# Kernel tuning notes

Hardware: AMD Instinct MI355X
Metric: run time of the kernel (lower is better)

The kernel has to match this reference:

```python
import jax, jax.numpy as jnp
import numpy as np

EPS = 1e-8


def setup_inputs() -> dict:
    key = jax.random.key(0)
    student_output = jax.random.normal(key, (8192, 768), dtype=jnp.float32)
    return {"student_output": student_output}


def reference(student_output) -> jnp.ndarray:
    # F.normalize(x, p=2, dim=-1, eps): x / max(||x||, eps)
    norm = jnp.linalg.norm(student_output, axis=-1, keepdims=True)
    x = student_output / jnp.maximum(norm, EPS)  # [B, D]

    # Brute-force 1-NN via max inner product (vectors are L2-normalized)
    dots = x @ x.T  # [B, B]
    n = x.shape[0]
    dots = dots.at[jnp.arange(n), jnp.arange(n)].set(-1.0)  # mask self
    indices = jnp.argmax(dots, axis=1)  # [B]

    # torch.nn.PairwiseDistance(2, eps): ||x1 - x2 + eps||_2
    diff = x - x[indices] + EPS  # [B, D]
    distances = jnp.sqrt(jnp.sum(diff * diff, axis=-1))  # [B]

    loss = -jnp.mean(jnp.log(distances + EPS))
    return loss
```

## Files before the change

### kernel.cpp

```cpp
#include <hip/hip_runtime.h>
#include <math.h>

#define NB 8192
#define D 768
#define EPSV 1e-8f
#define BT 256
#define BK 64
#define NT (NB / BT)
#define NBLK (NT * (NT + 1) / 2)

typedef float f32x4 __attribute__((ext_vector_type(4)));
typedef short s16x8 __attribute__((ext_vector_type(8)));

#define BARM() asm volatile("s_barrier" ::: "memory")
#define LGKM0() asm volatile("s_waitcnt lgkmcnt(0)" ::: "memory")
#define VMC(n) asm volatile("s_waitcnt vmcnt(" #n ")" ::: "memory")

__device__ __forceinline__ unsigned short f2bf(float f) {
  unsigned u = __float_as_uint(f);
  u += 0x7fffu + ((u >> 16) & 1u);
  return (unsigned short)(u >> 16);
}
__device__ __forceinline__ unsigned encf(float f) {
  unsigned u = __float_as_uint(f);
  return (u & 0x80000000u) ? ~u : (u | 0x80000000u);
}
__device__ __forceinline__ float decf(unsigned u) {
  return (u & 0x80000000u) ? __uint_as_float(u & 0x7fffffffu)
                           : __uint_as_float(~u);
}
__device__ __forceinline__ void mfma_bf16(f32x4& c, s16x8 a, s16x8 b) {
  c = __builtin_amdgcn_mfma_f32_16x16x32_bf16(a, b, c, 0, 0, 0);
}

__device__ __forceinline__ int swz(int p) { return p ^ (((p >> 7) & 7) << 4); }

__device__ __forceinline__ void stage_half(const unsigned short* __restrict__ xb,
                                           unsigned short* lds, int rbase,
                                           int row0, int k0, int w, int l) {
#pragma unroll
  for (int i = 0; i < 2; ++i) {
    const int pu = i * 8192 + w * 1024;
    const int p = pu + l * 16;
    const int sp = swz(p);
    const unsigned short* src =
        xb + (size_t)(row0 + (sp >> 7)) * D + k0 + ((sp & 127) >> 1);
    __builtin_amdgcn_global_load_lds(
        (const __attribute__((address_space(1))) void*)src,
        (__attribute__((address_space(3))) void*)(lds + rbase + (pu >> 1)), 16,
        0, 0);
  }
}

__device__ __forceinline__ s16x8 ldfrag(const unsigned short* lds, int rbase,
                                        int r, int c) {
  const int b = swz((r << 7) | (c << 1));
  return *(const s16x8*)(lds + rbase + (b >> 1));
}

__global__ __launch_bounds__(256) void normalize_kernel(
    const float* __restrict__ in, unsigned short* __restrict__ xb) {
  const int row = blockIdx.x;
  const int t = threadIdx.x;
  float4 v = make_float4(0.f, 0.f, 0.f, 0.f);
  const float4* rp = (const float4*)(in + (size_t)row * D);
  if (t < D / 4) v = rp[t];
  float ss = v.x * v.x + v.y * v.y + v.z * v.z + v.w * v.w;
#pragma unroll
  for (int m = 1; m < 64; m <<= 1) ss += __shfl_xor(ss, m, 64);
  __shared__ float wss[4];
  if ((t & 63) == 0) wss[t >> 6] = ss;
  __syncthreads();
  float tot = wss[0] + wss[1] + wss[2] + wss[3];
  float inv = 1.0f / fmaxf(sqrtf(tot), EPSV);
  if (t < D / 4) {
    ushort4 o;
    o.x = f2bf(v.x * inv);
    o.y = f2bf(v.y * inv);
    o.z = f2bf(v.z * inv);
    o.w = f2bf(v.w * inv);
    *(ushort4*)(xb + (size_t)row * D + t * 4) = o;
  }
}

__global__ __launch_bounds__(512) void gemm_max_kernel(
    const unsigned short* __restrict__ xb, unsigned* __restrict__ gmax) {
  __shared__ unsigned short lds[65536];
  const int t = threadIdx.x;
  const int w = t >> 6, l = t & 63;
  const int wm = w >> 2, wn = w & 3;

  const int bid = blockIdx.x;
  const int widx = (bid & 7) * (NBLK / 8) + (bid >> 3);
  int brow = (int)((sqrtf(8.0f * (float)widx + 1.0f) - 1.0f) * 0.5f);
  while ((brow + 1) * (brow + 2) / 2 <= widx) ++brow;
  while (brow * (brow + 1) / 2 > widx) --brow;
  const int bcol = widx - brow * (brow + 1) / 2;
  const bool diag = (brow == bcol);
  const int arow = brow * BT, acol = bcol * BT;

  f32x4 acc[8][4] = {};

  const int AB = wm * 8192;
  const int BB = 16384 + (wn >> 1) * 8192;

#define RD_B(buf)                                                             \
  {                                                                           \
    _Pragma("unroll") for (int n = 0; n < 4; ++n) _Pragma("unroll") for (     \
        int kk = 0; kk < 2;                                                   \
        ++kk) bfr[n * 2 + kk] = ldfrag(lds, (buf) + BB,                       \
                                       (wn & 1) * 64 + n * 16 + (l & 15),     \
                                       kk * 32 + (l >> 4) * 8);               \
  }
#define RD_A(buf, dst, m0)                                                    \
  {                                                                           \
    _Pragma("unroll") for (int mm = 0; mm < 2; ++mm) _Pragma("unroll") for (  \
        int kk = 0; kk < 2;                                                   \
        ++kk) dst[mm * 2 + kk] = ldfrag(lds, (buf) + AB,                      \
                                        ((m0) + mm) * 16 + (l & 15),          \
                                        kk * 32 + (l >> 4) * 8);              \
  }
#define MFMA_Q(q, a)                                                          \
  {                                                                           \
    __builtin_amdgcn_s_setprio(1);                                            \
    _Pragma("unroll") for (int mm = 0; mm < 2; ++mm)                          \
        _Pragma("unroll") for (int n = 0; n < 4; ++n)                         \
            _Pragma("unroll") for (int kk = 0; kk < 2; ++kk)                  \
                mfma_bf16(acc[2 * (q) + mm][n], a[mm * 2 + kk],               \
                          bfr[n * 2 + kk]);                                   \
    __builtin_amdgcn_s_setprio(0);                                            \
  }

  stage_half(xb, lds, 0, arow, 0, w, l);
  stage_half(xb, lds, 8192, arow + 128, 0, w, l);
  stage_half(xb, lds, 16384, acol, 0, w, l);
  stage_half(xb, lds, 24576, acol + 128, 0, w, l);
  VMC(4);
  stage_half(xb, lds, 32768 + 16384, acol, 64, w, l);
  stage_half(xb, lds, 32768 + 24576, acol + 128, 64, w, l);
  stage_half(xb, lds, 32768, arow, 64, w, l);
  VMC(6);
  BARM();

#pragma unroll 1
  for (int itn = 0; itn < 6; ++itn) {
    const int kC1 = 2 * itn + 1;
    const int kS0 = (2 * itn + 2 < 12) ? 2 * itn + 2 : 11;
    const int kS1 = (2 * itn + 3 < 12) ? 2 * itn + 3 : 11;
    s16x8 bfr[8], aA[4], aB[4], aC[4], aD[4];

    RD_B(0);
    RD_A(0, aA, 0);
    stage_half(xb, lds, 32768 + 8192, arow + 128, kC1 * 64, w, l);
    BARM();
    LGKM0();
    MFMA_Q(0, aA);
    BARM();

    RD_A(0, aB, 2);
    RD_A(0, aC, 4);
    stage_half(xb, lds, 16384, acol, kS0 * 64, w, l);
    BARM();
    LGKM0();
    MFMA_Q(1, aB);
    BARM();

    RD_A(0, aD, 6);
    stage_half(xb, lds, 24576, acol + 128, kS0 * 64, w, l);
    BARM();
    LGKM0();
    MFMA_Q(2, aC);
    BARM();

    stage_half(xb, lds, 0, arow, kS0 * 64, w, l);
    BARM();
    LGKM0();
    MFMA_Q(3, aD);
    VMC(6);
    BARM();

    RD_B(32768);
    RD_A(32768, aA, 0);
    stage_half(xb, lds, 8192, arow + 128, kS0 * 64, w, l);
    BARM();
    LGKM0();
    MFMA_Q(0, aA);
    BARM();

    RD_A(32768, aB, 2);
    RD_A(32768, aC, 4);
    stage_half(xb, lds, 32768 + 16384, acol, kS1 * 64, w, l);
    BARM();
    LGKM0();
    MFMA_Q(1, aB);
    BARM();

    RD_A(32768, aD, 6);
    stage_half(xb, lds, 32768 + 24576, acol + 128, kS1 * 64, w, l);
    BARM();
    LGKM0();
    MFMA_Q(2, aC);
    BARM();

    stage_half(xb, lds, 32768, arow, kS1 * 64, w, l);
    BARM();
    LGKM0();
    MFMA_Q(3, aD);
    VMC(6);
    BARM();
  }

  const int q4 = l >> 4, c0 = l & 15;
  const int rowbase = arow + wm * 128;
  const int colbase = acol + wn * 64;
#pragma unroll
  for (int m = 0; m < 8; ++m) {
#pragma unroll
    for (int reg = 0; reg < 4; ++reg) {
      const int grow = rowbase + m * 16 + q4 * 4 + reg;
      float v = -INFINITY;
#pragma unroll
      for (int n = 0; n < 4; ++n) {
        float val = acc[m][n][reg];
        if (diag && grow == colbase + n * 16 + c0) val = -1.0f;
        v = fmaxf(v, val);
      }
      v = fmaxf(v, __shfl_xor(v, 1));
      v = fmaxf(v, __shfl_xor(v, 2));
      v = fmaxf(v, __shfl_xor(v, 4));
      v = fmaxf(v, __shfl_xor(v, 8));
      if (c0 == 0) atomicMax(&gmax[grow], encf(v));
    }
  }
  if (!diag) {
#pragma unroll
    for (int n = 0; n < 4; ++n) {
      float v = -INFINITY;
#pragma unroll
      for (int m = 0; m < 8; ++m)
#pragma unroll
        for (int reg = 0; reg < 4; ++reg) v = fmaxf(v, acc[m][n][reg]);
      v = fmaxf(v, __shfl_xor(v, 16));
      v = fmaxf(v, __shfl_xor(v, 32));
      if (q4 == 0) atomicMax(&gmax[colbase + n * 16 + c0], encf(v));
    }
  }
  asm volatile("s_waitcnt vmcnt(0)" ::: "memory");
}

__global__ __launch_bounds__(1024) void loss_kernel(
    const unsigned* __restrict__ gmax, float* __restrict__ out) {
  const int t = threadIdx.x;
  float s = 0.f;
  for (int i = t; i < NB; i += 1024) {
    float dot = decf(gmax[i]);
    float d2 = fmaxf(2.0f - 2.0f * dot, 0.0f);
    s += logf(sqrtf(d2) + EPSV);
  }
#pragma unroll
  for (int m = 1; m < 64; m <<= 1) s += __shfl_xor(s, m, 64);
  __shared__ float wsum[16];
  if ((t & 63) == 0) wsum[t >> 6] = s;
  __syncthreads();
  if (t == 0) {
    float tot = 0.f;
#pragma unroll
    for (int i = 0; i < 16; ++i) tot += wsum[i];
    out[0] = -tot / (float)NB;
  }
}

extern "C" void kernel_launch(void* const* d_in, const int* in_sizes, int n_in,
                              void* d_out, int out_size, void* d_ws,
                              size_t ws_size, hipStream_t stream) {
  const float* in = (const float*)d_in[0];
  float* out = (float*)d_out;
  unsigned* gmax = (unsigned*)d_ws;
  unsigned short* xb = (unsigned short*)((char*)d_ws + 32768);

  hipMemsetAsync(gmax, 0, NB * sizeof(unsigned), stream);
  normalize_kernel<<<NB, 256, 0, stream>>>(in, xb);
  gemm_max_kernel<<<NBLK, 512, 0, stream>>>(xb, gmax);
  loss_kernel<<<1, 1024, 0, stream>>>(gmax, out);
}
```

Baseline: 127.6 us.

## Replace global atomicMax with per-tile partial maxima and parallel row reduction

Each GEMM tile now reduces its row and column maxima in LDS and writes one partial-max vector per tile to global buffers, replacing per-row global atomicMax on encoded floats. A new 32-block kernel reduces the partials per row block and computes the log-distance sums, and a tiny final kernel combines them, which also removes the memset and the single-block loss kernel. The aim is to cut atomic contention and serial tail work, at the cost of an extra launch and a little more global memory traffic.

```diff
diff --git a/kernel.cpp b/kernel.cpp
--- a/kernel.cpp
+++ b/kernel.cpp
@@ -20,14 +20,6 @@
   unsigned u = __float_as_uint(f);
   u += 0x7fffu + ((u >> 16) & 1u);
   return (unsigned short)(u >> 16);
-}
-__device__ __forceinline__ unsigned encf(float f) {
-  unsigned u = __float_as_uint(f);
-  return (u & 0x80000000u) ? ~u : (u | 0x80000000u);
-}
-__device__ __forceinline__ float decf(unsigned u) {
-  return (u & 0x80000000u) ? __uint_as_float(u & 0x7fffffffu)
-                           : __uint_as_float(~u);
 }
 __device__ __forceinline__ void mfma_bf16(f32x4& c, s16x8 a, s16x8 b) {
   c = __builtin_amdgcn_mfma_f32_16x16x32_bf16(a, b, c, 0, 0, 0);
@@ -84,7 +76,8 @@
 }
 
 __global__ __launch_bounds__(512) void gemm_max_kernel(
-    const unsigned short* __restrict__ xb, unsigned* __restrict__ gmax) {
+    const unsigned short* __restrict__ xb, float* __restrict__ P1,
+    float* __restrict__ P2) {
   __shared__ unsigned short lds[65536];
   const int t = threadIdx.x;
   const int w = t >> 6, l = t & 63;
@@ -210,26 +203,29 @@
     BARM();
   }
 
+  VMC(0);
+  BARM();
+  float* sr = (float*)lds;
+  float* sc = sr + 1024;
   const int q4 = l >> 4, c0 = l & 15;
-  const int rowbase = arow + wm * 128;
-  const int colbase = acol + wn * 64;
+
 #pragma unroll
   for (int m = 0; m < 8; ++m) {
 #pragma unroll
     for (int reg = 0; reg < 4; ++reg) {
-      const int grow = rowbase + m * 16 + q4 * 4 + reg;
+      const int lrow = wm * 128 + m * 16 + q4 * 4 + reg;
       float v = -INFINITY;
 #pragma unroll
       for (int n = 0; n < 4; ++n) {
         float val = acc[m][n][reg];
-        if (diag && grow == colbase + n * 16 + c0) val = -1.0f;
+        if (diag && lrow == wn * 64 + n * 16 + c0) val = -1.0f;
         v = fmaxf(v, val);
       }
       v = fmaxf(v, __shfl_xor(v, 1));
       v = fmaxf(v, __shfl_xor(v, 2));
       v = fmaxf(v, __shfl_xor(v, 4));
       v = fmaxf(v, __shfl_xor(v, 8));
-      if (c0 == 0) atomicMax(&gmax[grow], encf(v));
+      if (c0 == 0) sr[wn * 256 + lrow] = v;
     }
   }
   if (!diag) {
@@ -242,32 +238,43 @@
         for (int reg = 0; reg < 4; ++reg) v = fmaxf(v, acc[m][n][reg]);
       v = fmaxf(v, __shfl_xor(v, 16));
       v = fmaxf(v, __shfl_xor(v, 32));
-      if (q4 == 0) atomicMax(&gmax[colbase + n * 16 + c0], encf(v));
+      if (q4 == 0) sc[wm * 256 + wn * 64 + n * 16 + c0] = v;
     }
   }
-  asm volatile("s_waitcnt vmcnt(0)" ::: "memory");
-}
-
-__global__ __launch_bounds__(1024) void loss_kernel(
-    const unsigned* __restrict__ gmax, float* __restrict__ out) {
-  const int t = threadIdx.x;
-  float s = 0.f;
-  for (int i = t; i < NB; i += 1024) {
-    float dot = decf(gmax[i]);
-    float d2 = fmaxf(2.0f - 2.0f * dot, 0.0f);
-    s += logf(sqrtf(d2) + EPSV);
-  }
-#pragma unroll
-  for (int m = 1; m < 64; m <<= 1) s += __shfl_xor(s, m, 64);
-  __shared__ float wsum[16];
-  if ((t & 63) == 0) wsum[t >> 6] = s;
+  BARM();
+  if (t < 256) {
+    const float r = fmaxf(fmaxf(sr[t], sr[256 + t]),
+                          fmaxf(sr[512 + t], sr[768 + t]));
+    P1[(brow * 32 + bcol) * 256 + t] = r;
+    const float c = diag ? r : fmaxf(sc[t], sc[256 + t]);
+    P2[(bcol * 32 + brow) * 256 + t] = c;
+  }
+}
+
+__global__ __launch_bounds__(256) void rowdist_kernel(
+    const float* __restrict__ P1, const float* __restrict__ P2,
+    float* __restrict__ psum) {
+  const int R = blockIdx.x, j = threadIdx.x;
+  float m = -INFINITY;
+  for (int c = 0; c <= R; ++c) m = fmaxf(m, P1[(R * 32 + c) * 256 + j]);
+  for (int r = R; r < 32; ++r) m = fmaxf(m, P2[(R * 32 + r) * 256 + j]);
+  const float d2 = fmaxf(2.0f - 2.0f * m, 0.0f);
+  float s = logf(sqrtf(d2) + EPSV);
+#pragma unroll
+  for (int o = 1; o < 64; o <<= 1) s += __shfl_xor(s, o, 64);
+  __shared__ float ws4[4];
+  if ((j & 63) == 0) ws4[j >> 6] = s;
   __syncthreads();
-  if (t == 0) {
-    float tot = 0.f;
-#pragma unroll
-    for (int i = 0; i < 16; ++i) tot += wsum[i];
-    out[0] = -tot / (float)NB;
-  }
+  if (j == 0) psum[R] = ws4[0] + ws4[1] + ws4[2] + ws4[3];
+}
+
+__global__ __launch_bounds__(64) void final_kernel(
+    const float* __restrict__ psum, float* __restrict__ out) {
+  const int l = threadIdx.x;
+  float s = (l < 32) ? psum[l] : 0.0f;
+#pragma unroll
+  for (int o = 1; o < 64; o <<= 1) s += __shfl_xor(s, o, 64);
+  if (l == 0) out[0] = -s / (float)NB;
 }
 
 extern "C" void kernel_launch(void* const* d_in, const int* in_sizes, int n_in,
@@ -275,11 +282,13 @@
                               size_t ws_size, hipStream_t stream) {
   const float* in = (const float*)d_in[0];
   float* out = (float*)d_out;
-  unsigned* gmax = (unsigned*)d_ws;
-  unsigned short* xb = (unsigned short*)((char*)d_ws + 32768);
-
-  hipMemsetAsync(gmax, 0, NB * sizeof(unsigned), stream);
+  float* P1 = (float*)d_ws;
+  float* P2 = P1 + 32 * 32 * 256;
+  float* psum = P2 + 32 * 32 * 256;
+  unsigned short* xb = (unsigned short*)(psum + 64);
+
   normalize_kernel<<<NB, 256, 0, stream>>>(in, xb);
-  gemm_max_kernel<<<NBLK, 512, 0, stream>>>(xb, gmax);
-  loss_kernel<<<1, 1024, 0, stream>>>(gmax, out);
-}
+  gemm_max_kernel<<<NBLK, 512, 0, stream>>>(xb, P1, P2);
+  rowdist_kernel<<<32, 256, 0, stream>>>(P1, P2, psum);
+  final_kernel<<<1, 64, 0, stream>>>(psum, out);
+}
```

After: 121.3 us. -5.0%, faster.
